# Performance work log

Measured on AMD Instinct MI355X. Metric: run time of the kernel, lower is better.

## Reference

```python
import jax, jax.numpy as jnp
import numpy as np

EMBED = 64
OUT = 64
KERW = 64
DIM = 3

def setup_inputs() -> dict:
    key = jax.random.key(0)
    ks = jax.random.split(key, 6)
    x = jax.random.normal(ks[0], (8, 4096, EMBED), dtype=jnp.float32)
    grid = jax.random.uniform(ks[1], (8, 4096, DIM), dtype=jnp.float32)
    # DenseNet([dim, ker_width_l, output_size*embed_size], GELU): two Linear layers,
    # GELU between, no activation after the last layer.
    W1 = jax.random.normal(ks[2], (DIM, KERW), dtype=jnp.float32) / np.sqrt(DIM)
    b1 = jnp.zeros((KERW,), dtype=jnp.float32)
    W2 = jax.random.normal(ks[3], (KERW, OUT * EMBED), dtype=jnp.float32) / np.sqrt(KERW)
    b2 = jnp.zeros((OUT * EMBED,), dtype=jnp.float32)
    return {"x": x, "grid": grid, "W1": W1, "b1": b1, "W2": W2, "b2": b2}

def reference(x, grid, W1, b1, W2, b2):
    shape = x.shape
    # generator MLP: grid [.., dim] -> per-point weight [.., embed*out]
    h = jax.nn.gelu(grid @ W1 + b1, approximate=False)
    weight = h @ W2 + b2                              # [B, P, embed*out]
    weight = weight.reshape(-1, EMBED, OUT)           # [N, embed, out]
    xf = x.reshape(-1, shape[-1])                     # [N, embed]
    out = jnp.einsum('bi,bio->bo', xf, weight)        # [N, out]
    return out.reshape(*shape[:-1], OUT)
```

## Files before the change

kernel.cpp:

```cpp
#include <hip/hip_runtime.h>
#include <hip/hip_bf16.h>
#include <hip/hip_fp16.h>

typedef _Float16 f16x8 __attribute__((ext_vector_type(8)));
typedef float f32x4 __attribute__((ext_vector_type(4)));

#define N_PTS 32768
#define NCHUNK 65
#define ROWS 64
#define X_STRIDE 72
#define P_STRIDE 68

__global__ __launch_bounds__(256) void prep_kernel(
    const float* __restrict__ W2, const float* __restrict__ b2,
    _Float16* __restrict__ wsB) {
  __shared__ _Float16 w_lds[64][X_STRIDE];
  const int c   = blockIdx.x;
  const int tid = threadIdx.x;
  {
    const float* src = (c < 64) ? (W2 + c * 4096 + tid * 16) : (b2 + tid * 16);
    int kl = tid >> 2, o = (tid & 3) * 16;
    f16x8 v0, v1;
    #pragma unroll
    for (int j = 0; j < 8; ++j) {
      v0[j] = (_Float16)src[j];
      v1[j] = (_Float16)src[8 + j];
    }
    *(f16x8*)(&w_lds[kl][o])     = v0;
    *(f16x8*)(&w_lds[kl][o + 8]) = v1;
  }
  __syncthreads();
  #pragma unroll
  for (int u = 0; u < 2; ++u) {
    int t = tid + u * 256;
    int q = t >> 6, lane = t & 63;
    int klbase = (q >> 2) * 32 + ((lane >> 4) & 3) * 8;
    int o      = (q & 3) * 16 + (lane & 15);
    f16x8 v;
    #pragma unroll
    for (int j = 0; j < 8; ++j) v[j] = w_lds[klbase + j][o];
    *(f16x8*)(wsB + c * 4096 + t * 8) = v;
  }
}

__global__ __launch_bounds__(256) void main_kernel(
    const float* __restrict__ x, const float* __restrict__ gridp,
    const float* __restrict__ W1, const float* __restrict__ b1,
    const _Float16* __restrict__ wsB, float* __restrict__ out) {

  __shared__ _Float16 h_t[4][ROWS][16];
  __shared__ float part[4][ROWS * P_STRIDE];
  _Float16* x_lds = (_Float16*)&part[0][0];

  const int tid  = threadIdx.x;
  const int lane = tid & 63;
  const int wave = tid >> 6;
  const int rowblk = blockIdx.x * ROWS;

  const float* xsrc = x + rowblk * 64 + tid * 16;
  f32x4 xr0 = *(const f32x4*)(xsrc);
  f32x4 xr1 = *(const f32x4*)(xsrc + 4);
  f32x4 xr2 = *(const f32x4*)(xsrc + 8);
  f32x4 xr3 = *(const f32x4*)(xsrc + 12);

  {
    int row = tid >> 2;
    int w4  = tid & 3;
    int r = rowblk + row;
    float g0 = gridp[r * 3 + 0], g1 = gridp[r * 3 + 1], g2 = gridp[r * 3 + 2];
    f16x8 h0, h1;
    #pragma unroll
    for (int q = 0; q < 16; ++q) {
      int k = w4 + 4 * q;
      float v = g0 * W1[k] + g1 * W1[64 + k] + g2 * W1[128 + k] + b1[k];
      float h = 0.5f * v * (1.0f + erff(v * 0.7071067811865476f));
      if (q < 8) h0[q] = (_Float16)h; else h1[q - 8] = (_Float16)h;
    }
    *(f16x8*)(&h_t[w4][row][0]) = h0;
    *(f16x8*)(&h_t[w4][row][8]) = h1;
  }

  {
    int row = tid >> 2, o = (tid & 3) * 16;
    f16x8 v0, v1;
    #pragma unroll
    for (int j = 0; j < 4; ++j) {
      v0[j]     = (_Float16)xr0[j];
      v0[4 + j] = (_Float16)xr1[j];
      v1[j]     = (_Float16)xr2[j];
      v1[4 + j] = (_Float16)xr3[j];
    }
    *(f16x8*)(&x_lds[row * X_STRIDE + o])     = v0;
    *(f16x8*)(&x_lds[row * X_STRIDE + o + 8]) = v1;
  }
  __syncthreads();

  const int mrow = lane & 15;
  const int kgrp = lane >> 4;
  const _Float16* bp = wsB + lane * 8;

  auto LOADB = [&](f16x8* b, int c) {
    #pragma unroll
    for (int q = 0; q < 8; ++q)
      b[q] = *(const f16x8*)(bp + (c * 8 + q) * 512);
  };

  f16x8 bA[8], bB[8], bC[8];
  LOADB(bA, wave);
  LOADB(bB, wave + 4);
  LOADB(bC, wave + 8);

  f16x8 hreg[4][2];
  #pragma unroll
  for (int m = 0; m < 4; ++m) {
    hreg[m][0] = *(const f16x8*)(&h_t[wave][m * 16 + mrow][0]);
    hreg[m][1] = *(const f16x8*)(&h_t[wave][m * 16 + mrow][8]);
  }

  f16x8 xf[4][2];
  #pragma unroll
  for (int m = 0; m < 4; ++m)
    #pragma unroll
    for (int s = 0; s < 2; ++s)
      xf[m][s] = *(const f16x8*)(&x_lds[(m * 16 + mrow) * X_STRIDE + s * 32 + kgrp * 8]);

  f32x4 acc[4][4];
  #pragma unroll
  for (int m = 0; m < 4; ++m)
    #pragma unroll
    for (int n = 0; n < 4; ++n)
      acc[m][n] = (f32x4){0.f, 0.f, 0.f, 0.f};

  auto COMPUTE = [&](const f16x8* b, int p) {
    #pragma unroll
    for (int m = 0; m < 4; ++m) {
      _Float16 hh = hreg[m][p >> 3][p & 7];
      f16x8 hs = {hh, hh, hh, hh, hh, hh, hh, hh};
      f16x8 a0 = xf[m][0] * hs;
      f16x8 a1 = xf[m][1] * hs;
      #pragma unroll
      for (int n = 0; n < 4; ++n) {
        acc[m][n] = __builtin_amdgcn_mfma_f32_16x16x32_f16(a0, b[n],     acc[m][n], 0, 0, 0);
        acc[m][n] = __builtin_amdgcn_mfma_f32_16x16x32_f16(a1, b[4 + n], acc[m][n], 0, 0, 0);
      }
    }
  };
  auto COMPUTE_BIAS = [&](const f16x8* b) {
    #pragma unroll
    for (int m = 0; m < 4; ++m)
      #pragma unroll
      for (int n = 0; n < 4; ++n) {
        acc[m][n] = __builtin_amdgcn_mfma_f32_16x16x32_f16(xf[m][0], b[n],     acc[m][n], 0, 0, 0);
        acc[m][n] = __builtin_amdgcn_mfma_f32_16x16x32_f16(xf[m][1], b[4 + n], acc[m][n], 0, 0, 0);
      }
  };

  #pragma unroll
  for (int g = 0; g < 5; ++g) {
    COMPUTE(bA, 3 * g);
    if (3 * g + 3 < 16) LOADB(bA, wave + 4 * (3 * g + 3));
    COMPUTE(bB, 3 * g + 1);
    if (3 * g + 4 < 16) LOADB(bB, wave + 4 * (3 * g + 4));
    else if (wave == 0) LOADB(bB, 64);
    COMPUTE(bC, 3 * g + 2);
    if (3 * g + 5 < 16) LOADB(bC, wave + 4 * (3 * g + 5));
  }
  COMPUTE(bA, 15);
  if (wave == 0) COMPUTE_BIAS(bB);

  __syncthreads();

  {
    float* pw = part[wave];
    #pragma unroll
    for (int m = 0; m < 4; ++m)
      #pragma unroll
      for (int n = 0; n < 4; ++n)
        #pragma unroll
        for (int r = 0; r < 4; ++r)
          pw[(m * 16 + kgrp * 4 + r) * P_STRIDE + n * 16 + mrow] = acc[m][n][r];
  }
  __syncthreads();

  {
    int row = tid >> 2;
    int cb  = (tid & 3) * 16;
    const float* p0 = part[0] + row * P_STRIDE + cb;
    float* op = out + (rowblk + row) * 64 + cb;
    #pragma unroll
    for (int j = 0; j < 4; ++j) {
      f32x4 s = *(const f32x4*)(p0 + j * 4);
      #pragma unroll
      for (int w = 1; w < 4; ++w)
        s += *(const f32x4*)(p0 + w * (ROWS * P_STRIDE) + j * 4);
      *(f32x4*)(op + j * 4) = s;
    }
  }
}

extern "C" void kernel_launch(void* const* d_in, const int* in_sizes, int n_in,
                              void* d_out, int out_size, void* d_ws, size_t ws_size,
                              hipStream_t stream) {
  const float* x    = (const float*)d_in[0];
  const float* grid = (const float*)d_in[1];
  const float* W1   = (const float*)d_in[2];
  const float* b1   = (const float*)d_in[3];
  const float* W2   = (const float*)d_in[4];
  const float* b2   = (const float*)d_in[5];
  float* out = (float*)d_out;
  _Float16* wsB = (_Float16*)d_ws;

  hipLaunchKernelGGL(prep_kernel, dim3(NCHUNK), dim3(256), 0, stream,
                     W2, b2, wsB);
  hipLaunchKernelGGL(main_kernel, dim3(N_PTS / ROWS), dim3(256), 0, stream,
                     x, grid, W1, b1, wsB, out);
}
```

Measured before the change: 30.33 us.

## Switch to 32x32x16 MFMA with 2x2 wave split over K and N

Replaces the 16x16x32 MFMA tiling with 32x32x16 MFMA. Waves are split as two K-halves by two N-halves instead of four K-quarters, and the B-operand prep layout is reshaped to match. Each wave now loads half the B fragments per hidden index, and the cross-wave reduction drops from four partial buffers to two, cutting LDS traffic and register pressure. The exact erf GELU is replaced by a tanh-style approximation using exp2 and a hardware reciprocal, which risks small accuracy differences.

Result: slower. 32.24 us (+6.3%).

```diff
diff --git a/kernel.cpp b/kernel.cpp
--- a/kernel.cpp
+++ b/kernel.cpp
@@ -1,20 +1,17 @@
 #include <hip/hip_runtime.h>
-#include <hip/hip_bf16.h>
 #include <hip/hip_fp16.h>
 
 typedef _Float16 f16x8 __attribute__((ext_vector_type(8)));
 typedef float f32x4 __attribute__((ext_vector_type(4)));
+typedef float f32x16 __attribute__((ext_vector_type(16)));
 
 #define N_PTS 32768
-#define NCHUNK 65
 #define ROWS 64
-#define X_STRIDE 72
-#define P_STRIDE 68
 
 __global__ __launch_bounds__(256) void prep_kernel(
     const float* __restrict__ W2, const float* __restrict__ b2,
     _Float16* __restrict__ wsB) {
-  __shared__ _Float16 w_lds[64][X_STRIDE];
+  __shared__ _Float16 w_lds[64][72];
   const int c   = blockIdx.x;
   const int tid = threadIdx.x;
   {
@@ -33,9 +30,11 @@
   #pragma unroll
   for (int u = 0; u < 2; ++u) {
     int t = tid + u * 256;
-    int q = t >> 6, lane = t & 63;
-    int klbase = (q >> 2) * 32 + ((lane >> 4) & 3) * 8;
-    int o      = (q & 3) * 16 + (lane & 15);
+    int lane = t & 63;
+    int kt   = (t >> 6) & 3;
+    int ns   = t >> 8;
+    int klbase = kt * 16 + ((lane >> 5) << 3);
+    int o      = ns * 32 + (lane & 31);
     f16x8 v;
     #pragma unroll
     for (int j = 0; j < 8; ++j) v[j] = w_lds[klbase + j][o];
@@ -48,14 +47,18 @@
     const float* __restrict__ W1, const float* __restrict__ b1,
     const _Float16* __restrict__ wsB, float* __restrict__ out) {
 
-  __shared__ _Float16 h_t[4][ROWS][16];
-  __shared__ float part[4][ROWS * P_STRIDE];
-  _Float16* x_lds = (_Float16*)&part[0][0];
+  __shared__ float part[2][ROWS][68];
+  __shared__ _Float16 h_t[2][4][ROWS][8];
+  _Float16* x_lds = (_Float16*)&part[0][0][0];
 
   const int tid  = threadIdx.x;
   const int lane = tid & 63;
   const int wave = tid >> 6;
+  const int ks   = wave & 1;
+  const int ns   = wave >> 1;
   const int rowblk = blockIdx.x * ROWS;
+  const int r31 = lane & 31;
+  const int hi  = lane >> 5;
 
   const float* xsrc = x + rowblk * 64 + tid * 16;
   f32x4 xr0 = *(const f32x4*)(xsrc);
@@ -64,20 +67,27 @@
   f32x4 xr3 = *(const f32x4*)(xsrc + 12);
 
   {
-    int row = tid >> 2;
-    int w4  = tid & 3;
+    int row = tid >> 2, sub = tid & 3;
     int r = rowblk + row;
     float g0 = gridp[r * 3 + 0], g1 = gridp[r * 3 + 1], g2 = gridp[r * 3 + 2];
-    f16x8 h0, h1;
+    f16x8 he, ho;
     #pragma unroll
     for (int q = 0; q < 16; ++q) {
-      int k = w4 + 4 * q;
+      int k = sub * 16 + q;
       float v = g0 * W1[k] + g1 * W1[64 + k] + g2 * W1[128 + k] + b1[k];
-      float h = 0.5f * v * (1.0f + erff(v * 0.7071067811865476f));
-      if (q < 8) h0[q] = (_Float16)h; else h1[q - 8] = (_Float16)h;
-    }
-    *(f16x8*)(&h_t[w4][row][0]) = h0;
-    *(f16x8*)(&h_t[w4][row][8]) = h1;
+      float v2 = v * v;
+      float pp = fmaf(0.044715f, v2, 1.0f);
+      float u  = v * pp;
+      float e  = exp2f(u * 2.3022084f);
+      float rr = e + 1.0f;
+      float inv;
+      asm("v_rcp_f32 %0, %1" : "=v"(inv) : "v"(rr));
+      float h = v * (1.0f - inv);
+      if ((q & 1) == 0) he[q >> 1] = (_Float16)h;
+      else              ho[q >> 1] = (_Float16)h;
+    }
+    *(f16x8*)(&h_t[0][sub][row][0]) = he;
+    *(f16x8*)(&h_t[1][sub][row][0]) = ho;
   }
 
   {
@@ -90,109 +100,99 @@
       v1[j]     = (_Float16)xr2[j];
       v1[4 + j] = (_Float16)xr3[j];
     }
-    *(f16x8*)(&x_lds[row * X_STRIDE + o])     = v0;
-    *(f16x8*)(&x_lds[row * X_STRIDE + o + 8]) = v1;
-  }
-  __syncthreads();
-
-  const int mrow = lane & 15;
-  const int kgrp = lane >> 4;
+    *(f16x8*)(&x_lds[row * 72 + o])     = v0;
+    *(f16x8*)(&x_lds[row * 72 + o + 8]) = v1;
+  }
+  __syncthreads();
+
   const _Float16* bp = wsB + lane * 8;
 
   auto LOADB = [&](f16x8* b, int c) {
     #pragma unroll
-    for (int q = 0; q < 8; ++q)
-      b[q] = *(const f16x8*)(bp + (c * 8 + q) * 512);
+    for (int kt = 0; kt < 4; ++kt)
+      b[kt] = *(const f16x8*)(bp + (c * 8 + ns * 4 + kt) * 512);
   };
 
-  f16x8 bA[8], bB[8], bC[8];
-  LOADB(bA, wave);
-  LOADB(bB, wave + 4);
-  LOADB(bC, wave + 8);
-
-  f16x8 hreg[4][2];
-  #pragma unroll
-  for (int m = 0; m < 4; ++m) {
-    hreg[m][0] = *(const f16x8*)(&h_t[wave][m * 16 + mrow][0]);
-    hreg[m][1] = *(const f16x8*)(&h_t[wave][m * 16 + mrow][8]);
-  }
-
-  f16x8 xf[4][2];
-  #pragma unroll
-  for (int m = 0; m < 4; ++m)
-    #pragma unroll
-    for (int s = 0; s < 2; ++s)
-      xf[m][s] = *(const f16x8*)(&x_lds[(m * 16 + mrow) * X_STRIDE + s * 32 + kgrp * 8]);
-
-  f32x4 acc[4][4];
-  #pragma unroll
-  for (int m = 0; m < 4; ++m)
-    #pragma unroll
-    for (int n = 0; n < 4; ++n)
-      acc[m][n] = (f32x4){0.f, 0.f, 0.f, 0.f};
+  f16x8 bA[4], bB[4], bC[4];
+  LOADB(bA, ks);
+  LOADB(bB, ks + 2);
+  LOADB(bC, ks + 4);
+
+  f16x8 hreg[2][4];
+  #pragma unroll
+  for (int mt = 0; mt < 2; ++mt)
+    #pragma unroll
+    for (int ph = 0; ph < 4; ++ph)
+      hreg[mt][ph] = *(const f16x8*)(&h_t[ks][ph][mt * 32 + r31][0]);
+
+  f16x8 xf[2][4];
+  #pragma unroll
+  for (int mt = 0; mt < 2; ++mt)
+    #pragma unroll
+    for (int kt = 0; kt < 4; ++kt)
+      xf[mt][kt] = *(const f16x8*)(&x_lds[(mt * 32 + r31) * 72 + kt * 16 + hi * 8]);
+
+  f32x16 acc[2];
+  #pragma unroll
+  for (int mt = 0; mt < 2; ++mt)
+    #pragma unroll
+    for (int i = 0; i < 16; ++i) acc[mt][i] = 0.f;
 
   auto COMPUTE = [&](const f16x8* b, int p) {
     #pragma unroll
-    for (int m = 0; m < 4; ++m) {
-      _Float16 hh = hreg[m][p >> 3][p & 7];
+    for (int mt = 0; mt < 2; ++mt) {
+      _Float16 hh = hreg[mt][p >> 3][p & 7];
       f16x8 hs = {hh, hh, hh, hh, hh, hh, hh, hh};
-      f16x8 a0 = xf[m][0] * hs;
-      f16x8 a1 = xf[m][1] * hs;
       #pragma unroll
-      for (int n = 0; n < 4; ++n) {
-        acc[m][n] = __builtin_amdgcn_mfma_f32_16x16x32_f16(a0, b[n],     acc[m][n], 0, 0, 0);
-        acc[m][n] = __builtin_amdgcn_mfma_f32_16x16x32_f16(a1, b[4 + n], acc[m][n], 0, 0, 0);
-      }
+      for (int kt = 0; kt < 4; ++kt)
+        acc[mt] = __builtin_amdgcn_mfma_f32_32x32x16_f16(xf[mt][kt] * hs, b[kt],
+                                                         acc[mt], 0, 0, 0);
     }
   };
   auto COMPUTE_BIAS = [&](const f16x8* b) {
     #pragma unroll
-    for (int m = 0; m < 4; ++m)
+    for (int mt = 0; mt < 2; ++mt)
       #pragma unroll
-      for (int n = 0; n < 4; ++n) {
-        acc[m][n] = __builtin_amdgcn_mfma_f32_16x16x32_f16(xf[m][0], b[n],     acc[m][n], 0, 0, 0);
-        acc[m][n] = __builtin_amdgcn_mfma_f32_16x16x32_f16(xf[m][1], b[4 + n], acc[m][n], 0, 0, 0);
+      for (int kt = 0; kt < 4; ++kt)
+        acc[mt] = __builtin_amdgcn_mfma_f32_32x32x16_f16(xf[mt][kt], b[kt],
+                                                         acc[mt], 0, 0, 0);
+  };
+
+  #pragma unroll
+  for (int g = 0; g < 10; ++g) {
+    COMPUTE(bA, 3 * g);
+    if (3 * g + 3 < 32) LOADB(bA, ks + 2 * (3 * g + 3));
+    COMPUTE(bB, 3 * g + 1);
+    if (3 * g + 4 < 32) LOADB(bB, ks + 2 * (3 * g + 4));
+    COMPUTE(bC, 3 * g + 2);
+    if (3 * g + 5 < 32)      LOADB(bC, ks + 2 * (3 * g + 5));
+    else if (3 * g + 5 == 32 && ks == 0) LOADB(bC, 64);
+  }
+  COMPUTE(bA, 30);
+  COMPUTE(bB, 31);
+  if (ks == 0) COMPUTE_BIAS(bC);
+
+  __syncthreads();
+
+  {
+    #pragma unroll
+    for (int mt = 0; mt < 2; ++mt)
+      #pragma unroll
+      for (int r = 0; r < 16; ++r) {
+        int rowL = mt * 32 + (r & 3) + 8 * (r >> 2) + 4 * hi;
+        part[ks][rowL][ns * 32 + r31] = acc[mt][r];
       }
-  };
-
-  #pragma unroll
-  for (int g = 0; g < 5; ++g) {
-    COMPUTE(bA, 3 * g);
-    if (3 * g + 3 < 16) LOADB(bA, wave + 4 * (3 * g + 3));
-    COMPUTE(bB, 3 * g + 1);
-    if (3 * g + 4 < 16) LOADB(bB, wave + 4 * (3 * g + 4));
-    else if (wave == 0) LOADB(bB, 64);
-    COMPUTE(bC, 3 * g + 2);
-    if (3 * g + 5 < 16) LOADB(bC, wave + 4 * (3 * g + 5));
-  }
-  COMPUTE(bA, 15);
-  if (wave == 0) COMPUTE_BIAS(bB);
-
-  __syncthreads();
-
-  {
-    float* pw = part[wave];
-    #pragma unroll
-    for (int m = 0; m < 4; ++m)
-      #pragma unroll
-      for (int n = 0; n < 4; ++n)
-        #pragma unroll
-        for (int r = 0; r < 4; ++r)
-          pw[(m * 16 + kgrp * 4 + r) * P_STRIDE + n * 16 + mrow] = acc[m][n][r];
   }
   __syncthreads();
 
   {
     int row = tid >> 2;
     int cb  = (tid & 3) * 16;
-    const float* p0 = part[0] + row * P_STRIDE + cb;
     float* op = out + (rowblk + row) * 64 + cb;
     #pragma unroll
     for (int j = 0; j < 4; ++j) {
-      f32x4 s = *(const f32x4*)(p0 + j * 4);
-      #pragma unroll
-      for (int w = 1; w < 4; ++w)
-        s += *(const f32x4*)(p0 + w * (ROWS * P_STRIDE) + j * 4);
+      f32x4 s = *(const f32x4*)(&part[0][row][cb + j * 4]);
+      s += *(const f32x4*)(&part[1][row][cb + j * 4]);
       *(f32x4*)(op + j * 4) = s;
     }
   }
@@ -210,7 +210,7 @@
   float* out = (float*)d_out;
   _Float16* wsB = (_Float16*)d_ws;
 
-  hipLaunchKernelGGL(prep_kernel, dim3(NCHUNK), dim3(256), 0, stream,
+  hipLaunchKernelGGL(prep_kernel, dim3(65), dim3(256), 0, stream,
                      W2, b2, wsB);
   hipLaunchKernelGGL(main_kernel, dim3(N_PTS / ROWS), dim3(256), 0, stream,
                      x, grid, W1, b1, wsB, out);
```
